# Optimization experiments

Hardware: AMD Instinct MI355X
Metric: run time of the kernel (lower is better)

The kernel has to match this reference:

```python
import jax, jax.numpy as jnp
import numpy as np

N, D, R, E = 10000, 1024, 8, 80000


def setup_inputs() -> dict:
    key = jax.random.key(0)
    ks = jax.random.split(key, 8)
    s = 1.0 / np.sqrt(D)
    x = jax.random.normal(ks[0], (N, D), dtype=jnp.float32)
    edge_index = jax.random.randint(ks[1], (2, E), 0, N, dtype=jnp.int64)
    edge_type = jax.random.randint(ks[2], (E,), 0, R, dtype=jnp.int64)
    weight = jax.random.normal(ks[3], (R, D, D), dtype=jnp.float32) * s  # per-relation W_r
    root = jax.random.normal(ks[4], (D, D), dtype=jnp.float32) * s      # root/self-loop weight
    bias = jnp.zeros((D,), dtype=jnp.float32)
    w_gate = jax.random.normal(ks[5], (2 * D, D), dtype=jnp.float32) * (1.0 / np.sqrt(2 * D))
    b_gate = jnp.zeros((D,), dtype=jnp.float32)
    return {"x": x, "edge_index": edge_index, "edge_type": edge_type,
            "weight": weight, "root": root, "bias": bias,
            "w_gate": w_gate, "b_gate": b_gate}


def _rgcn(x, edge_index, edge_type, weight, root, bias):
    # PyG RGCNConv (aggr='mean'): per relation r, mean-aggregate x[src] into dst,
    # then transform by W_r (aggregate-then-transform, equivalent by linearity).
    src, dst = edge_index[0], edge_index[1]
    msgs = x[src]                                   # [E, D] gather
    out = x @ root + bias                           # root/self connection
    n = x.shape[0]
    for r in range(weight.shape[0]):                # small fixed relation loop
        mask = (edge_type == r).astype(x.dtype)     # [E]
        sums = jax.ops.segment_sum(msgs * mask[:, None], dst, num_segments=n)
        cnt = jax.ops.segment_sum(mask, dst, num_segments=n)
        mean = sums / jnp.maximum(cnt, 1.0)[:, None]
        out = out + mean @ weight[r]
    return out


def reference(x, edge_index, edge_type, weight, root, bias, w_gate, b_gate):
    u = _rgcn(x, edge_index, edge_type, weight, root, bias)
    # dropout p=0 -> identity
    z = jnp.concatenate([u, x], axis=1) @ w_gate + b_gate
    h = jnp.tanh(u) * z + x * (1.0 - z)
    return h
```

## Files before the change

### kernel.cpp

```cpp
#include <hip/hip_runtime.h>
#include <math.h>

typedef unsigned short u16;
typedef __attribute__((ext_vector_type(8))) short bf16x8;
typedef __attribute__((ext_vector_type(4))) float f32x4;

static constexpr int kN = 10000;
static constexpr int kNpad = 10240;
static constexpr int kD = 1024;
static constexpr int kR = 8;
static constexpr int kE = 80000;
static constexpr int kKz = 2 * kD;
static constexpr int kCrows = kNpad * (kR + 1);
static constexpr int kTilesY = kCrows / 256;

#define GLB(p) ((const __attribute__((address_space(1))) unsigned int*)(const void*)(p))
#define LDSP(p) ((__attribute__((address_space(3))) unsigned int*)(p))

__device__ __forceinline__ u16 f2bf(float f) {
    union { float f; unsigned int i; } c; c.f = f;
    unsigned int u = c.i;
    return (u16)((u + 0x7FFFu + ((u >> 16) & 1u)) >> 16);
}
__device__ __forceinline__ float bf2f(u16 u) {
    union { unsigned int i; float f; } c; c.i = ((unsigned int)u) << 16;
    return c.f;
}
__device__ __forceinline__ ushort4 f2bf4(float4 v) {
    ushort4 o; o.x = f2bf(v.x); o.y = f2bf(v.y); o.z = f2bf(v.z); o.w = f2bf(v.w);
    return o;
}

__global__ void zero16(uint4* __restrict__ p, long n16) {
    long i = (long)blockIdx.x * blockDim.x + threadIdx.x;
    long st = (long)gridDim.x * blockDim.x;
    uint4 z = make_uint4(0, 0, 0, 0);
    for (; i < n16; i += st) p[i] = z;
}

__global__ void mark_edges(const int* __restrict__ src, const int* __restrict__ dst,
                           const int* __restrict__ etype,
                           int* __restrict__ cntd, int* __restrict__ flag) {
    int e = blockIdx.x * blockDim.x + threadIdx.x;
    if (e < kE) {
        atomicAdd(&cntd[dst[e]], 1);
        flag[etype[e] * kN + src[e]] = 1;
    }
}

__global__ __launch_bounds__(1024) void scan_rowptr(const int* __restrict__ cnt,
                                                    int* __restrict__ rowptr,
                                                    int* __restrict__ cursor) {
    __shared__ int wsum[16];
    __shared__ int carry;
    const int tid = threadIdx.x;
    const int lane = tid & 63;
    const int w = tid >> 6;
    if (tid == 0) carry = 0;
    const int nchunk = (kN + 1024) / 1024;
    for (int ch = 0; ch < nchunk; ++ch) {
        int idx = ch * 1024 + tid;
        int v = (idx < kN) ? cnt[idx] : 0;
        int s = v;
#pragma unroll
        for (int off = 1; off < 64; off <<= 1) {
            int t = __shfl_up(s, off, 64);
            if (lane >= off) s += t;
        }
        if (lane == 63) wsum[w] = s;
        __syncthreads();
        if (w == 0 && lane < 16) {
            int t = wsum[lane];
#pragma unroll
            for (int off = 1; off < 16; off <<= 1) {
                int tt = __shfl_up(t, off, 64);
                if (lane >= off) t += tt;
            }
            wsum[lane] = t;
        }
        __syncthreads();
        int wpre = (w > 0) ? wsum[w - 1] : 0;
        int incl = s + wpre + carry;
        int excl = incl - v;
        if (idx <= kN) rowptr[idx] = excl;
        if (idx < kN) cursor[idx] = 0;
        __syncthreads();
        if (tid == 1023) carry = incl;
        __syncthreads();
    }
}

__global__ __launch_bounds__(1024) void compact_scan(const int* __restrict__ flag,
                                                     int* __restrict__ row_src,
                                                     int* __restrict__ pos_tab,
                                                     int* __restrict__ relcnt9) {
    const int tid = threadIdx.x;
    if (blockIdx.x == kR) {
        for (int i = tid; i < kNpad; i += 1024) row_src[i] = i;
        if (tid == 0) relcnt9[0] = kN;
        return;
    }
    const int r = blockIdx.x;
    const int base = kNpad * (r + 1);
    __shared__ int wsum[16];
    __shared__ int carry;
    const int lane = tid & 63;
    const int w = tid >> 6;
    if (tid == 0) carry = 0;
    const int nchunk = (kN + 1023) / 1024;
    for (int ch = 0; ch < nchunk; ++ch) {
        int idx = ch * 1024 + tid;
        int v = (idx < kN) ? flag[r * kN + idx] : 0;
        int s = v;
#pragma unroll
        for (int off = 1; off < 64; off <<= 1) {
            int t = __shfl_up(s, off, 64);
            if (lane >= off) s += t;
        }
        if (lane == 63) wsum[w] = s;
        __syncthreads();
        if (w == 0 && lane < 16) {
            int t = wsum[lane];
#pragma unroll
            for (int off = 1; off < 16; off <<= 1) {
                int tt = __shfl_up(t, off, 64);
                if (lane >= off) t += tt;
            }
            wsum[lane] = t;
        }
        __syncthreads();
        int wpre = (w > 0) ? wsum[w - 1] : 0;
        int incl = s + wpre + carry;
        int excl = incl - v;
        if (idx < kN && v) {
            row_src[base + excl] = idx;
            pos_tab[r * kN + idx] = base + excl;
        }
        __syncthreads();
        if (tid == 1023) carry = incl;
        __syncthreads();
    }
    if (tid == 0) relcnt9[r + 1] = carry;
}

__global__ void fill_edges(const int* __restrict__ src, const int* __restrict__ dst,
                           const int* __restrict__ etype, const int* __restrict__ rowptr,
                           int* __restrict__ cursor, const int* __restrict__ pos_tab,
                           int* __restrict__ erec) {
    int e = blockIdx.x * blockDim.x + threadIdx.x;
    if (e < kE) {
        int d = dst[e], r = etype[e], s = src[e];
        int pos = rowptr[d] + atomicAdd(&cursor[d], 1);
        erec[pos] = (pos_tab[r * kN + s] << 3) | r;
    }
}

__global__ void cvt_x(const float* __restrict__ x, u16* __restrict__ ga) {
    int row = blockIdx.x;
    int c = threadIdx.x << 2;
    float4 v = *reinterpret_cast<const float4*>(x + (size_t)row * kD + c);
    *reinterpret_cast<ushort4*>(ga + (size_t)row * kKz + kD + c) = f2bf4(v);
}

__global__ void transpose_to_bf16(const float* __restrict__ S, u16* __restrict__ D,
                                  int rows, int cols, int ldD) {
    S += (size_t)blockIdx.z * rows * cols;
    D += (size_t)blockIdx.z * rows * cols;
    __shared__ float t[32][33];
    int c0 = blockIdx.x * 32, r0 = blockIdx.y * 32;
    int x = threadIdx.x, y = threadIdx.y;
#pragma unroll
    for (int i = 0; i < 32; i += 8)
        t[y + i][x] = S[(size_t)(r0 + y + i) * cols + c0 + x];
    __syncthreads();
#pragma unroll
    for (int i = 0; i < 32; i += 8)
        D[(size_t)(c0 + y + i) * ldD + r0 + x] = f2bf(t[x][y + i]);
}

__global__ __launch_bounds__(256) void aggregate(const u16* __restrict__ yc,
                                                 const float* __restrict__ bias,
                                                 const int* __restrict__ rowptr,
                                                 const int* __restrict__ erec,
                                                 u16* __restrict__ ga) {
    const int d = blockIdx.x;
    const int c = threadIdx.x << 2;
    const int e0 = rowptr[d], e1 = rowptr[d + 1];

    __shared__ float rs[kR];
    if (threadIdx.x == 0) {
        int cc[kR] = {0, 0, 0, 0, 0, 0, 0, 0};
        for (int e = e0; e < e1; ++e) cc[erec[e] & 7]++;
#pragma unroll
        for (int r = 0; r < kR; ++r) rs[r] = 1.0f / fmaxf((float)cc[r], 1.0f);
    }
    __syncthreads();

    ushort4 rv = *reinterpret_cast<const ushort4*>(yc + (size_t)d * kD + c);
    float4 bv = *reinterpret_cast<const float4*>(bias + c);
    float4 acc = make_float4(bf2f(rv.x) + bv.x, bf2f(rv.y) + bv.y,
                             bf2f(rv.z) + bv.z, bf2f(rv.w) + bv.w);

    int e = e0;
    for (; e + 1 < e1; e += 2) {
        int rec0 = erec[e];
        int rec1 = erec[e + 1];
        ushort4 v0 = *reinterpret_cast<const ushort4*>(yc + (size_t)(rec0 >> 3) * kD + c);
        ushort4 v1 = *reinterpret_cast<const ushort4*>(yc + (size_t)(rec1 >> 3) * kD + c);
        float s0 = rs[rec0 & 7];
        float s1 = rs[rec1 & 7];
        acc.x += s0 * bf2f(v0.x); acc.y += s0 * bf2f(v0.y);
        acc.z += s0 * bf2f(v0.z); acc.w += s0 * bf2f(v0.w);
        acc.x += s1 * bf2f(v1.x); acc.y += s1 * bf2f(v1.y);
        acc.z += s1 * bf2f(v1.z); acc.w += s1 * bf2f(v1.w);
    }
    if (e < e1) {
        int rec = erec[e];
        float sc = rs[rec & 7];
        ushort4 v = *reinterpret_cast<const ushort4*>(yc + (size_t)(rec >> 3) * kD + c);
        acc.x += sc * bf2f(v.x); acc.y += sc * bf2f(v.y);
        acc.z += sc * bf2f(v.z); acc.w += sc * bf2f(v.w);
    }
    *reinterpret_cast<ushort4*>(ga + (size_t)d * kKz + c) = f2bf4(acc);
}

__global__ __launch_bounds__(256, 2) void gemm_compact(
    const u16* __restrict__ xb, int ldx,
    const u16* __restrict__ Bt9,
    const int* __restrict__ row_src, const int* __restrict__ relcnt9,
    u16* __restrict__ yc)
{
    const int t = blockIdx.y;
    const int relidx = t / 40;
    const int lt = t - relidx * 40;
    if (lt * 256 >= relcnt9[relidx]) return;

    __shared__ u16 sA[256 * 32];
    __shared__ u16 sB[128 * 32];

    const int tid = threadIdx.x;
    const int wave = tid >> 6;
    const int lane = tid & 63;

    const int row0 = t * 256;
    const int col0 = blockIdx.x * 128;

    const int srow4 = lane >> 2;
    const int scol = (lane & 3) * 8;

    const u16* gA[4];
    u16* lA[4];
#pragma unroll
    for (int q = 0; q < 4; ++q) {
        int r = wave * 64 + q * 16;
        int srcrow = row_src[row0 + r + srow4];
        gA[q] = xb + (size_t)srcrow * ldx + scol;
        lA[q] = sA + r * 32;
    }
    const u16* gB[2];
    u16* lB[2];
#pragma unroll
    for (int p = 0; p < 2; ++p) {
        int r = p * 64 + wave * 16;
        gB[p] = Bt9 + (size_t)(relidx * kD + col0 + r + srow4) * kD + scol;
        lB[p] = sB + r * 32;
    }

    const int mq = (wave >> 1) * 128;
    const int nq = (wave & 1) * 64;
    const int fm = lane & 15;
    const int fk = (lane >> 4) * 8;

    f32x4 zf = {0.0f, 0.0f, 0.0f, 0.0f};
    f32x4 acc[8][4];
#pragma unroll
    for (int i = 0; i < 8; ++i)
#pragma unroll
        for (int j = 0; j < 4; ++j) acc[i][j] = zf;

    for (int k0 = 0; k0 < kD; k0 += 32) {
        __syncthreads();
#pragma unroll
        for (int q = 0; q < 4; ++q)
            __builtin_amdgcn_global_load_lds(GLB(gA[q]), LDSP(lA[q]), 16, 0, 0);
#pragma unroll
        for (int p = 0; p < 2; ++p)
            __builtin_amdgcn_global_load_lds(GLB(gB[p]), LDSP(lB[p]), 16, 0, 0);
#pragma unroll
        for (int q = 0; q < 4; ++q) gA[q] += 32;
#pragma unroll
        for (int p = 0; p < 2; ++p) gB[p] += 32;
        __syncthreads();

        bf16x8 af[8], bfr[4];
#pragma unroll
        for (int i = 0; i < 8; ++i)
            af[i] = *reinterpret_cast<const bf16x8*>(&sA[(mq + i * 16 + fm) * 32 + fk]);
#pragma unroll
        for (int j = 0; j < 4; ++j)
            bfr[j] = *reinterpret_cast<const bf16x8*>(&sB[(nq + j * 16 + fm) * 32 + fk]);
#pragma unroll
        for (int i = 0; i < 8; ++i)
#pragma unroll
            for (int j = 0; j < 4; ++j)
                acc[i][j] = __builtin_amdgcn_mfma_f32_16x16x32_bf16(bfr[j], af[i], acc[i][j], 0, 0, 0);
    }

    const int cq = (lane >> 4) * 4;
#pragma unroll
    for (int i = 0; i < 8; ++i) {
        int row = row0 + mq + i * 16 + fm;
#pragma unroll
        for (int j = 0; j < 4; ++j) {
            int col = col0 + nq + j * 16 + cq;
            f32x4 v = acc[i][j];
            ushort4 o;
            o.x = f2bf(v[0]); o.y = f2bf(v[1]); o.z = f2bf(v[2]); o.w = f2bf(v[3]);
            *reinterpret_cast<ushort4*>(yc + (size_t)row * kD + col) = o;
        }
    }
}

__global__ __launch_bounds__(256) void gemm_mfma_gate(
    const u16* __restrict__ A, int lda,
    const u16* __restrict__ Bt, int ldb, int K,
    int M, const float* __restrict__ bias,
    float* __restrict__ Cf, const u16* __restrict__ uga, const float* __restrict__ xo)
{
    __shared__ u16 sA[128 * 32];
    __shared__ u16 sB[128 * 32];

    const int tid = threadIdx.x;
    const int wave = tid >> 6;
    const int lane = tid & 63;

    constexpr int GX = kD / 128;
    constexpr int GY = kNpad / 128;
    const int lin = blockIdx.y * GX + blockIdx.x;
    const int xcd = lin & 7;
    const int pos = lin >> 3;
    const int ty = xcd * (GY / 8) + (pos >> 3);
    const int tx = pos & 7;

    const int row0 = ty * 128;
    const int col0 = tx * 128;

    const int srow = wave * 16 + (lane >> 2);
    const int scol = (lane & 3) * 8;

    const u16* gA0 = A + (size_t)(row0 + srow) * lda + scol;
    const u16* gA1 = A + (size_t)(row0 + 64 + srow) * lda + scol;
    const u16* gB0 = Bt + (size_t)(col0 + srow) * ldb + scol;
    const u16* gB1 = Bt + (size_t)(col0 + 64 + srow) * ldb + scol;

    u16* lA0 = sA + (wave * 16) * 32;
    u16* lA1 = sA + (64 + wave * 16) * 32;
    u16* lB0 = sB + (wave * 16) * 32;
    u16* lB1 = sB + (64 + wave * 16) * 32;

    const int mq = (wave >> 1) * 64;
    const int nq = (wave & 1) * 64;
    const int fm = lane & 15;
    const int fk = (lane >> 4) * 8;

    f32x4 zf = {0.0f, 0.0f, 0.0f, 0.0f};
    f32x4 acc[4][4];
#pragma unroll
    for (int i = 0; i < 4; ++i)
#pragma unroll
        for (int j = 0; j < 4; ++j) acc[i][j] = zf;

    for (int k0 = 0; k0 < K; k0 += 32) {
        __syncthreads();
        __builtin_amdgcn_global_load_lds(GLB(gA0), LDSP(lA0), 16, 0, 0);
        __builtin_amdgcn_global_load_lds(GLB(gA1), LDSP(lA1), 16, 0, 0);
        __builtin_amdgcn_global_load_lds(GLB(gB0), LDSP(lB0), 16, 0, 0);
        __builtin_amdgcn_global_load_lds(GLB(gB1), LDSP(lB1), 16, 0, 0);
        gA0 += 32; gA1 += 32; gB0 += 32; gB1 += 32;
        __syncthreads();

        bf16x8 af[4], bfr[4];
#pragma unroll
        for (int i = 0; i < 4; ++i)
            af[i] = *reinterpret_cast<const bf16x8*>(&sA[(mq + i * 16 + fm) * 32 + fk]);
#pragma unroll
        for (int j = 0; j < 4; ++j)
            bfr[j] = *reinterpret_cast<const bf16x8*>(&sB[(nq + j * 16 + fm) * 32 + fk]);
#pragma unroll
        for (int i = 0; i < 4; ++i)
#pragma unroll
            for (int j = 0; j < 4; ++j)
                acc[i][j] = __builtin_amdgcn_mfma_f32_16x16x32_bf16(bfr[j], af[i], acc[i][j], 0, 0, 0);
    }

    const int cq = (lane >> 4) * 4;
#pragma unroll
    for (int i = 0; i < 4; ++i) {
        int row = row0 + mq + i * 16 + fm;
        if (row >= M) continue;
#pragma unroll
        for (int j = 0; j < 4; ++j) {
            int col = col0 + nq + j * 16 + cq;
            f32x4 v = acc[i][j];
            float4 bv = *reinterpret_cast<const float4*>(bias + col);
            v[0] += bv.x; v[1] += bv.y; v[2] += bv.z; v[3] += bv.w;
            ushort4 ur = *reinterpret_cast<const ushort4*>(uga + (size_t)row * kKz + col);
            float4 xr = *reinterpret_cast<const float4*>(xo + (size_t)row * kD + col);
            float4 h;
            h.x = tanhf(bf2f(ur.x)) * v[0] + xr.x * (1.0f - v[0]);
            h.y = tanhf(bf2f(ur.y)) * v[1] + xr.y * (1.0f - v[1]);
            h.z = tanhf(bf2f(ur.z)) * v[2] + xr.z * (1.0f - v[2]);
            h.w = tanhf(bf2f(ur.w)) * v[3] + xr.w * (1.0f - v[3]);
            *reinterpret_cast<float4*>(Cf + (size_t)row * kD + col) = h;
        }
    }
}

extern "C" void kernel_launch(void* const* d_in, const int* in_sizes, int n_in,
                              void* d_out, int out_size, void* d_ws, size_t ws_size,
                              hipStream_t stream) {
    (void)in_sizes; (void)n_in; (void)out_size; (void)ws_size;

    const float* x     = (const float*)d_in[0];
    const int* eidx    = (const int*)d_in[1];
    const int* etype   = (const int*)d_in[2];
    const float* weight= (const float*)d_in[3];
    const float* root  = (const float*)d_in[4];
    const float* bias  = (const float*)d_in[5];
    const float* wgate = (const float*)d_in[6];
    const float* bgate = (const float*)d_in[7];
    float* out = (float*)d_out;

    const int* src = eidx;
    const int* dst = eidx + kE;

    char* ws = (char*)d_ws;
    size_t off = 0;
    u16* yc   = (u16*)(ws + off);    off += (size_t)kCrows * kD * 2;
    u16* ga   = (u16*)(ws + off);    off += (size_t)kNpad * kKz * 2;
    u16* Bt9  = (u16*)(ws + off);    off += (size_t)(kR + 1) * kD * kD * 2;
    u16* wg_t = (u16*)(ws + off);    off += (size_t)kD * kKz * 2;
    int* cntd    = (int*)(ws + off); off += (size_t)kN * 4;
    int* flag    = (int*)(ws + off); off += (size_t)kR * kN * 4;
    int* row_src = (int*)(ws + off); off += (size_t)kCrows * 4;
    int* pos_tab = (int*)(ws + off); off += (size_t)kR * kN * 4;
    int* rowp    = (int*)(ws + off); off += (size_t)(kN + 16) * 4;
    int* curs    = (int*)(ws + off); off += (size_t)kN * 4;
    int* erec    = (int*)(ws + off); off += (size_t)kE * 4;
    int* relcnt9 = (int*)(ws + off); off += 16 * 4;

    zero16<<<180, 256, 0, stream>>>((uint4*)cntd, (long)(kN + kR * kN + kCrows) / 4);

    mark_edges<<<(kE + 255) / 256, 256, 0, stream>>>(src, dst, etype, cntd, flag);
    scan_rowptr<<<1, 1024, 0, stream>>>(cntd, rowp, curs);
    compact_scan<<<kR + 1, 1024, 0, stream>>>(flag, row_src, pos_tab, relcnt9);
    fill_edges<<<(kE + 255) / 256, 256, 0, stream>>>(src, dst, etype, rowp, curs,
                                                     pos_tab, erec);

    zero16<<<256, 256, 0, stream>>>((uint4*)(ga + (size_t)kN * kKz),
                                    (long)(kNpad - kN) * kKz * 2 / 16);

    cvt_x<<<kN, 256, 0, stream>>>(x, ga);

    {
        dim3 b(32, 8);
        transpose_to_bf16<<<dim3(kD / 32, kD / 32, 1), b, 0, stream>>>(root, Bt9, kD, kD, kD);
        transpose_to_bf16<<<dim3(kD / 32, kD / 32, kR), b, 0, stream>>>(
            weight, Bt9 + (size_t)kD * kD, kD, kD, kD);
        transpose_to_bf16<<<dim3(kD / 32, kKz / 32, 1), b, 0, stream>>>(wgate, wg_t, kKz, kD, kKz);
    }

    dim3 g1(kD / 128, kTilesY);
    gemm_compact<<<g1, 256, 0, stream>>>(ga + kD, kKz, Bt9, row_src, relcnt9, yc);

    aggregate<<<kN, 256, 0, stream>>>(yc, bias, rowp, erec, ga);

    dim3 g2(kD / 128, kNpad / 128);
    gemm_mfma_gate<<<g2, 256, 0, stream>>>(ga, kKz, wg_t, kKz, kKz, kN, bgate, out, ga, x);
}
```

Measured before the change: 487.0 us.

## Double-buffer LDS in both GEMMs and shrink compact GEMM tile to 128 rows

Both MFMA GEMM kernels switch to double-buffered shared memory, issuing the next K-slice's global-to-LDS loads before computing on the current slice, with one barrier per iteration. This hides global load latency behind MFMA work. The compact relation GEMM also drops from 256x128 to 128x128 tiles with finer per-relation early-exit granularity, and both kernels request 3 blocks per CU. The trade-off is less reuse per tile, more LDS per block and more register pressure from the occupancy hint.

Result: no change. 478.2 us (-1.8%).

```diff
diff --git a/kernel.cpp b/kernel.cpp
--- a/kernel.cpp
+++ b/kernel.cpp
@@ -12,7 +12,7 @@
 static constexpr int kE = 80000;
 static constexpr int kKz = 2 * kD;
 static constexpr int kCrows = kNpad * (kR + 1);
-static constexpr int kTilesY = kCrows / 256;
+static constexpr int kTilesY1 = kCrows / 128;
 
 #define GLB(p) ((const __attribute__((address_space(1))) unsigned int*)(const void*)(p))
 #define LDSP(p) ((__attribute__((address_space(3))) unsigned int*)(p))
@@ -224,91 +224,91 @@
     *reinterpret_cast<ushort4*>(ga + (size_t)d * kKz + c) = f2bf4(acc);
 }
 
-__global__ __launch_bounds__(256, 2) void gemm_compact(
+__global__ __launch_bounds__(256, 3) void gemm_compact(
     const u16* __restrict__ xb, int ldx,
     const u16* __restrict__ Bt9,
     const int* __restrict__ row_src, const int* __restrict__ relcnt9,
     u16* __restrict__ yc)
 {
     const int t = blockIdx.y;
-    const int relidx = t / 40;
-    const int lt = t - relidx * 40;
-    if (lt * 256 >= relcnt9[relidx]) return;
-
-    __shared__ u16 sA[256 * 32];
-    __shared__ u16 sB[128 * 32];
+    const int relidx = t / 80;
+    const int lt = t - relidx * 80;
+    if (lt * 128 >= relcnt9[relidx]) return;
+
+    __shared__ u16 sA[2][128 * 32];
+    __shared__ u16 sB[2][128 * 32];
 
     const int tid = threadIdx.x;
     const int wave = tid >> 6;
     const int lane = tid & 63;
 
-    const int row0 = t * 256;
+    const int row0 = t * 128;
     const int col0 = blockIdx.x * 128;
 
-    const int srow4 = lane >> 2;
+    const int srow = wave * 16 + (lane >> 2);
     const int scol = (lane & 3) * 8;
 
-    const u16* gA[4];
-    u16* lA[4];
-#pragma unroll
-    for (int q = 0; q < 4; ++q) {
-        int r = wave * 64 + q * 16;
-        int srcrow = row_src[row0 + r + srow4];
-        gA[q] = xb + (size_t)srcrow * ldx + scol;
-        lA[q] = sA + r * 32;
-    }
-    const u16* gB[2];
-    u16* lB[2];
-#pragma unroll
-    for (int p = 0; p < 2; ++p) {
-        int r = p * 64 + wave * 16;
-        gB[p] = Bt9 + (size_t)(relidx * kD + col0 + r + srow4) * kD + scol;
-        lB[p] = sB + r * 32;
-    }
-
-    const int mq = (wave >> 1) * 128;
+    const u16* gA0 = xb + (size_t)row_src[row0 + srow] * ldx + scol;
+    const u16* gA1 = xb + (size_t)row_src[row0 + 64 + srow] * ldx + scol;
+    const u16* gB0 = Bt9 + (size_t)(relidx * kD + col0 + srow) * kD + scol;
+    const u16* gB1 = Bt9 + (size_t)(relidx * kD + col0 + 64 + srow) * kD + scol;
+
+    const int lofA0 = (wave * 16) * 32;
+    const int lofA1 = (64 + wave * 16) * 32;
+
+    const int mq = (wave >> 1) * 64;
     const int nq = (wave & 1) * 64;
     const int fm = lane & 15;
     const int fk = (lane >> 4) * 8;
 
     f32x4 zf = {0.0f, 0.0f, 0.0f, 0.0f};
-    f32x4 acc[8][4];
-#pragma unroll
-    for (int i = 0; i < 8; ++i)
+    f32x4 acc[4][4];
+#pragma unroll
+    for (int i = 0; i < 4; ++i)
 #pragma unroll
         for (int j = 0; j < 4; ++j) acc[i][j] = zf;
 
+    __builtin_amdgcn_global_load_lds(GLB(gA0), LDSP(sA[0] + lofA0), 16, 0, 0);
+    __builtin_amdgcn_global_load_lds(GLB(gA1), LDSP(sA[0] + lofA1), 16, 0, 0);
+    __builtin_amdgcn_global_load_lds(GLB(gB0), LDSP(sB[0] + lofA0), 16, 0, 0);
+    __builtin_amdgcn_global_load_lds(GLB(gB1), LDSP(sB[0] + lofA1), 16, 0, 0);
+    gA0 += 32; gA1 += 32; gB0 += 32; gB1 += 32;
+    __syncthreads();
+
+    int cur = 0;
     for (int k0 = 0; k0 < kD; k0 += 32) {
-        __syncthreads();
-#pragma unroll
-        for (int q = 0; q < 4; ++q)
-            __builtin_amdgcn_global_load_lds(GLB(gA[q]), LDSP(lA[q]), 16, 0, 0);
-#pragma unroll
-        for (int p = 0; p < 2; ++p)
-            __builtin_amdgcn_global_load_lds(GLB(gB[p]), LDSP(lB[p]), 16, 0, 0);
-#pragma unroll
-        for (int q = 0; q < 4; ++q) gA[q] += 32;
-#pragma unroll
-        for (int p = 0; p < 2; ++p) gB[p] += 32;
-        __syncthreads();
-
-        bf16x8 af[8], bfr[4];
-#pragma unroll
-        for (int i = 0; i < 8; ++i)
-            af[i] = *reinterpret_cast<const bf16x8*>(&sA[(mq + i * 16 + fm) * 32 + fk]);
+        if (k0 + 32 < kD) {
+            u16* dA = sA[cur ^ 1];
+            u16* dB = sB[cur ^ 1];
+            __builtin_amdgcn_global_load_lds(GLB(gA0), LDSP(dA + lofA0), 16, 0, 0);
+            __builtin_amdgcn_global_load_lds(GLB(gA1), LDSP(dA + lofA1), 16, 0, 0);
+            __builtin_amdgcn_global_load_lds(GLB(gB0), LDSP(dB + lofA0), 16, 0, 0);
+            __builtin_amdgcn_global_load_lds(GLB(gB1), LDSP(dB + lofA1), 16, 0, 0);
+            gA0 += 32; gA1 += 32; gB0 += 32; gB1 += 32;
+        }
+
+        const u16* cA = sA[cur];
+        const u16* cB = sB[cur];
+        bf16x8 af[4], bfr[4];
+#pragma unroll
+        for (int i = 0; i < 4; ++i)
+            af[i] = *reinterpret_cast<const bf16x8*>(&cA[(mq + i * 16 + fm) * 32 + fk]);
 #pragma unroll
         for (int j = 0; j < 4; ++j)
-            bfr[j] = *reinterpret_cast<const bf16x8*>(&sB[(nq + j * 16 + fm) * 32 + fk]);
-#pragma unroll
-        for (int i = 0; i < 8; ++i)
+            bfr[j] = *reinterpret_cast<const bf16x8*>(&cB[(nq + j * 16 + fm) * 32 + fk]);
+#pragma unroll
+        for (int i = 0; i < 4; ++i)
 #pragma unroll
             for (int j = 0; j < 4; ++j)
                 acc[i][j] = __builtin_amdgcn_mfma_f32_16x16x32_bf16(bfr[j], af[i], acc[i][j], 0, 0, 0);
+
+        __syncthreads();
+        cur ^= 1;
     }
 
     const int cq = (lane >> 4) * 4;
 #pragma unroll
-    for (int i = 0; i < 8; ++i) {
+    for (int i = 0; i < 4; ++i) {
         int row = row0 + mq + i * 16 + fm;
 #pragma unroll
         for (int j = 0; j < 4; ++j) {
@@ -321,14 +321,14 @@
     }
 }
 
-__global__ __launch_bounds__(256) void gemm_mfma_gate(
+__global__ __launch_bounds__(256, 3) void gemm_mfma_gate(
     const u16* __restrict__ A, int lda,
     const u16* __restrict__ Bt, int ldb, int K,
     int M, const float* __restrict__ bias,
     float* __restrict__ Cf, const u16* __restrict__ uga, const float* __restrict__ xo)
 {
-    __shared__ u16 sA[128 * 32];
-    __shared__ u16 sB[128 * 32];
+    __shared__ u16 sA[2][128 * 32];
+    __shared__ u16 sB[2][128 * 32];
 
     const int tid = threadIdx.x;
     const int wave = tid >> 6;
@@ -353,10 +353,8 @@
     const u16* gB0 = Bt + (size_t)(col0 + srow) * ldb + scol;
     const u16* gB1 = Bt + (size_t)(col0 + 64 + srow) * ldb + scol;
 
-    u16* lA0 = sA + (wave * 16) * 32;
-    u16* lA1 = sA + (64 + wave * 16) * 32;
-    u16* lB0 = sB + (wave * 16) * 32;
-    u16* lB1 = sB + (64 + wave * 16) * 32;
+    const int lof0 = (wave * 16) * 32;
+    const int lof1 = (64 + wave * 16) * 32;
 
     const int mq = (wave >> 1) * 64;
     const int nq = (wave & 1) * 64;
@@ -370,27 +368,42 @@
 #pragma unroll
         for (int j = 0; j < 4; ++j) acc[i][j] = zf;
 
+    __builtin_amdgcn_global_load_lds(GLB(gA0), LDSP(sA[0] + lof0), 16, 0, 0);
+    __builtin_amdgcn_global_load_lds(GLB(gA1), LDSP(sA[0] + lof1), 16, 0, 0);
+    __builtin_amdgcn_global_load_lds(GLB(gB0), LDSP(sB[0] + lof0), 16, 0, 0);
+    __builtin_amdgcn_global_load_lds(GLB(gB1), LDSP(sB[0] + lof1), 16, 0, 0);
+    gA0 += 32; gA1 += 32; gB0 += 32; gB1 += 32;
+    __syncthreads();
+
+    int cur = 0;
     for (int k0 = 0; k0 < K; k0 += 32) {
-        __syncthreads();
-        __builtin_amdgcn_global_load_lds(GLB(gA0), LDSP(lA0), 16, 0, 0);
-        __builtin_amdgcn_global_load_lds(GLB(gA1), LDSP(lA1), 16, 0, 0);
-        __builtin_amdgcn_global_load_lds(GLB(gB0), LDSP(lB0), 16, 0, 0);
-        __builtin_amdgcn_global_load_lds(GLB(gB1), LDSP(lB1), 16, 0, 0);
-        gA0 += 32; gA1 += 32; gB0 += 32; gB1 += 32;
-        __syncthreads();
-
+        if (k0 + 32 < K) {
+            u16* dA = sA[cur ^ 1];
+            u16* dB = sB[cur ^ 1];
+            __builtin_amdgcn_global_load_lds(GLB(gA0), LDSP(dA + lof0), 16, 0, 0);
+            __builtin_amdgcn_global_load_lds(GLB(gA1), LDSP(dA + lof1), 16, 0, 0);
+            __builtin_amdgcn_global_load_lds(GLB(gB0), LDSP(dB + lof0), 16, 0, 0);
+            __builtin_amdgcn_global_load_lds(GLB(gB1), LDSP(dB + lof1), 16, 0, 0);
+            gA0 += 32; gA1 += 32; gB0 += 32; gB1 += 32;
+        }
+
+        const u16* cA = sA[cur];
+        const u16* cB = sB[cur];
         bf16x8 af[4], bfr[4];
 #pragma unroll
         for (int i = 0; i < 4; ++i)
-            af[i] = *reinterpret_cast<const bf16x8*>(&sA[(mq + i * 16 + fm) * 32 + fk]);
+            af[i] = *reinterpret_cast<const bf16x8*>(&cA[(mq + i * 16 + fm) * 32 + fk]);
 #pragma unroll
         for (int j = 0; j < 4; ++j)
-            bfr[j] = *reinterpret_cast<const bf16x8*>(&sB[(nq + j * 16 + fm) * 32 + fk]);
+            bfr[j] = *reinterpret_cast<const bf16x8*>(&cB[(nq + j * 16 + fm) * 32 + fk]);
 #pragma unroll
         for (int i = 0; i < 4; ++i)
 #pragma unroll
             for (int j = 0; j < 4; ++j)
                 acc[i][j] = __builtin_amdgcn_mfma_f32_16x16x32_bf16(bfr[j], af[i], acc[i][j], 0, 0, 0);
+
+        __syncthreads();
+        cur ^= 1;
     }
 
     const int cq = (lane >> 4) * 4;
@@ -470,7 +483,7 @@
         transpose_to_bf16<<<dim3(kD / 32, kKz / 32, 1), b, 0, stream>>>(wgate, wg_t, kKz, kD, kKz);
     }
 
-    dim3 g1(kD / 128, kTilesY);
+    dim3 g1(kD / 128, kTilesY1);
     gemm_compact<<<g1, 256, 0, stream>>>(ga + kD, kKz, Bt9, row_src, relcnt9, yc);
 
     aggregate<<<kN, 256, 0, stream>>>(yc, bias, rowp, erec, ga);
```
